# Kernel tuning notes

Measured on AMD Instinct MI355X. Metric: run time of the kernel, lower is better.

Reference implementation:

```python
import jax, jax.numpy as jnp
import numpy as np
from jax import lax

TF_ALPHA = 0.125


def _teacher_force(z, x, alpha):
    # z: (B, dz), x: (B, dx); force first dx dims of z where x is not NaN
    dx = x.shape[-1]
    head = z[:, :dx]
    forced = jnp.where(jnp.isnan(x), head, alpha * x + (1.0 - alpha) * head)
    return jnp.concatenate([forced, z[:, dx:]], axis=-1)


def setup_inputs() -> dict:
    key = jax.random.key(0)
    ks = jax.random.split(key, 8)
    B, T, dx, dz, dh, ds = 256, 1024, 64, 128, 512, 16
    X = jax.random.normal(ks[0], (B, T, dx), dtype=jnp.float32)
    inputs = jax.random.normal(ks[1], (B, T, ds), dtype=jnp.float32)
    # A in (0, 0.9) for stable linear part; small weight scales to avoid blowup over T steps
    A = jax.random.uniform(ks[2], (B, dz), dtype=jnp.float32) * 0.9
    W1 = jax.random.normal(ks[3], (B, dz, dh), dtype=jnp.float32) * (0.5 / np.sqrt(dh))
    W2 = jax.random.normal(ks[4], (B, dh, dz), dtype=jnp.float32) * (0.5 / np.sqrt(dz))
    h1 = jax.random.normal(ks[5], (B, dz), dtype=jnp.float32) * 0.1
    h2 = jax.random.normal(ks[6], (B, dh), dtype=jnp.float32) * 0.1
    C = jax.random.normal(ks[7], (B, dz, ds), dtype=jnp.float32) * (0.5 / np.sqrt(ds))
    return {"X": X, "inputs": inputs, "A": A, "W1": W1, "W2": W2,
            "h1": h1, "h2": h2, "C": C}


def _plrnn_forward(X, inputs, A, W1, W2, h1, h2, C):
    B, T, dx = X.shape
    dz = A.shape[-1]
    # z0 = zeros teacher-forced with alpha=1 from X[:, 0]
    z0 = jnp.zeros((B, dz), dtype=X.dtype)
    z0 = _teacher_force(z0, X[:, 0], alpha=1.0)

    Xt = jnp.transpose(X, (1, 0, 2))        # (T, B, dx)
    St = jnp.transpose(inputs, (1, 0, 2))   # (T, B, ds)

    def step(z, xs):
        x_t, s_t = xs
        zf = _teacher_force(z, x_t, TF_ALPHA)
        pre = jnp.einsum('bhz,bz->bh', W2, zf) + h2          # (B, dh)
        z_new = (A * zf
                 + jnp.einsum('bzh,bh->bz', W1, jax.nn.relu(pre))
                 + h1
                 + jnp.einsum('bzs,bs->bz', C, s_t))
        return z_new, z_new

    _, Z = lax.scan(step, z0, (Xt, St))      # Z: (T, B, dz)
    Z = jnp.transpose(Z, (1, 0, 2))          # (B, T, dz)
    return Z[:, :, :dx]                      # dim_x_proj == 0 path


def reference(X, inputs, A, W1, W2, h1, h2, C):
    return _plrnn_forward(X, inputs, A, W1, W2, h1, h2, C)
```

## Files before the change

### kernel.cpp

```cpp
#include <hip/hip_runtime.h>
#include <math.h>


#define NB 256
#define T  1024
#define DX 64
#define DZ 128
#define DH 512
#define DS 16
#define CHUNK 128

typedef _Float16 half8 __attribute__((ext_vector_type(8)));
typedef _Float16 v4h   __attribute__((ext_vector_type(4)));
typedef float    f32x4 __attribute__((ext_vector_type(4)));

__device__ __forceinline__ half8 cvt8(const float* __restrict__ src) {
  const float4 a = *reinterpret_cast<const float4*>(src);
  const float4 c = *reinterpret_cast<const float4*>(src + 4);
  half8 h;
  h[0] = (_Float16)a.x; h[1] = (_Float16)a.y; h[2] = (_Float16)a.z; h[3] = (_Float16)a.w;
  h[4] = (_Float16)c.x; h[5] = (_Float16)c.y; h[6] = (_Float16)c.z; h[7] = (_Float16)c.w;
  return h;
}

__global__ __launch_bounds__(512, 2) void plrnn_kernel(
    const float* __restrict__ X, const float* __restrict__ S,
    const float* __restrict__ A, const float* __restrict__ W1,
    const float* __restrict__ W2, const float* __restrict__ h1,
    const float* __restrict__ h2, const float* __restrict__ C,
    float* __restrict__ out)
{
  __shared__ __align__(16) _Float16 zf_h[DZ];
  __shared__ __align__(16) _Float16 rt[DH];
  __shared__ __align__(16) float    Xc[CHUNK][DX];
  __shared__ __align__(16) float    Sc[CHUNK][DS];
  __shared__ __align__(16) float    outc[CHUNK][DX];

  const int b   = blockIdx.x;
  const int tid = threadIdx.x;
  const int w   = tid >> 6;
  const int l   = tid & 63;
  const int g   = l >> 4;
  const int r15 = l & 15;

  {
    #pragma unroll
    for (int k = 0; k < 4; ++k) {
      const int flat = k * 2048 + tid * 4;
      int srow = 1 + (flat >> 6);
      if (srow > T - 1) srow = T - 1;
      const float4 v = *reinterpret_cast<const float4*>(X + ((size_t)b * T + srow) * DX + (flat & 63));
      *reinterpret_cast<float4*>(&((float*)Xc)[flat]) = v;
    }
    const int flat = tid * 4;
    const float4 v = *reinterpret_cast<const float4*>(S + ((size_t)b * T) * DS + flat);
    *reinterpret_cast<float4*>(&((float*)Sc)[flat]) = v;
  }

  half8 w2f[4][4];
  #pragma unroll
  for (int mt = 0; mt < 4; ++mt)
    #pragma unroll
    for (int kt = 0; kt < 4; ++kt)
      w2f[mt][kt] = cvt8(W2 + ((size_t)b * DH + 64 * w + 16 * mt + r15) * DZ + 32 * kt + 8 * g);

  half8 w1f[16];
  #pragma unroll
  for (int j = 0; j < 16; ++j) {
    const int kt = (2 * w + j) & 15;
    w1f[j] = cvt8(W1 + ((size_t)b * DZ + 16 * w + r15) * DH + 32 * kt + 8 * g);
  }

  half8 w1ft;
  #pragma unroll
  for (int e = 0; e < 8; ++e) w1ft[e] = (_Float16)0.0f;
  {
    const int row = 16 * w + r15;
    if (g == 0)      w1ft = cvt8(C + ((size_t)b * DZ + row) * DS + 0);
    else if (g == 1) w1ft = cvt8(C + ((size_t)b * DZ + row) * DS + 8);
  }

  f32x4 h2v[4];
  #pragma unroll
  for (int mt = 0; mt < 4; ++mt)
    h2v[mt] = *reinterpret_cast<const f32x4*>(h2 + (size_t)b * DH + 64 * w + 16 * mt + 4 * g);

  f32x4 Areg = {0.f, 0.f, 0.f, 0.f}, h1reg = {0.f, 0.f, 0.f, 0.f};
  f32x4 zfcur = {0.f, 0.f, 0.f, 0.f};
  if (r15 == 0) {
    Areg  = *reinterpret_cast<const f32x4*>(A  + (size_t)b * DZ + 16 * w + 4 * g);
    h1reg = *reinterpret_cast<const f32x4*>(h1 + (size_t)b * DZ + 16 * w + 4 * g);
    if (w < 4) {
      const f32x4 x0 = *reinterpret_cast<const f32x4*>(X + ((size_t)b * T) * DX + 16 * w + 4 * g);
      #pragma unroll
      for (int j = 0; j < 4; ++j) zfcur[j] = (x0[j] != x0[j]) ? 0.f : x0[j];
    }
    v4h zp;
    #pragma unroll
    for (int j = 0; j < 4; ++j) zp[j] = (_Float16)zfcur[j];
    *reinterpret_cast<v4h*>(&zf_h[16 * w + 4 * g]) = zp;
  }
  __syncthreads();

  const f32x4 zero4 = {0.f, 0.f, 0.f, 0.f};

  for (int t = 0; t < T; ++t) {
    if ((t & (CHUNK - 1)) == 0 && t) {
      const int c0 = t - CHUNK;
      #pragma unroll
      for (int k = 0; k < 4; ++k) {
        const int flat = k * 2048 + tid * 4;
        const float4 v = *reinterpret_cast<const float4*>(&((float*)outc)[flat]);
        *reinterpret_cast<float4*>(out + ((size_t)b * T + c0) * DX + flat) = v;
      }
      #pragma unroll
      for (int k = 0; k < 4; ++k) {
        const int flat = k * 2048 + tid * 4;
        int srow = t + 1 + (flat >> 6);
        if (srow > T - 1) srow = T - 1;
        const float4 v = *reinterpret_cast<const float4*>(X + ((size_t)b * T + srow) * DX + (flat & 63));
        *reinterpret_cast<float4*>(&((float*)Xc)[flat]) = v;
      }
      {
        const int flat = tid * 4;
        const float4 v = *reinterpret_cast<const float4*>(S + ((size_t)b * T + t) * DS + flat);
        *reinterpret_cast<float4*>(&((float*)Sc)[flat]) = v;
      }
      __syncthreads();
    }
    const int tc = t & (CHUNK - 1);

    const f32x4 xv  = *reinterpret_cast<const f32x4*>(&Xc[tc][16 * (w & 3) + 4 * g]);
    const f32x4 sa0 = *reinterpret_cast<const f32x4*>(&Sc[tc][8 * (g & 1)]);
    const f32x4 sa1 = *reinterpret_cast<const f32x4*>(&Sc[tc][8 * (g & 1) + 4]);
    half8 brt;
    #pragma unroll
    for (int e = 0; e < 4; ++e) {
      brt[e]     = (g < 2) ? (_Float16)sa0[e] : (_Float16)0.0f;
      brt[e + 4] = (g < 2) ? (_Float16)sa1[e] : (_Float16)0.0f;
    }
    const f32x4 tailv = __builtin_amdgcn_mfma_f32_16x16x32_f16(w1ft, brt, zero4, 0, 0, 0);

    half8 bz[4];
    #pragma unroll
    for (int kt = 0; kt < 4; ++kt)
      bz[kt] = *reinterpret_cast<const half8*>(zf_h + 32 * kt + 8 * g);

    f32x4 acc1[4];
    #pragma unroll
    for (int mt = 0; mt < 4; ++mt)
      acc1[mt] = __builtin_amdgcn_mfma_f32_16x16x32_f16(w2f[mt][0], bz[0], h2v[mt], 0, 0, 0);
    #pragma unroll
    for (int kt = 1; kt < 4; ++kt)
      #pragma unroll
      for (int mt = 0; mt < 4; ++mt)
        acc1[mt] = __builtin_amdgcn_mfma_f32_16x16x32_f16(w2f[mt][kt], bz[kt], acc1[mt], 0, 0, 0);

    if (r15 == 0) {
      #pragma unroll
      for (int mt = 0; mt < 4; ++mt) {
        v4h p;
        p[0] = (_Float16)fmaxf(acc1[mt][0], 0.f);
        p[1] = (_Float16)fmaxf(acc1[mt][1], 0.f);
        p[2] = (_Float16)fmaxf(acc1[mt][2], 0.f);
        p[3] = (_Float16)fmaxf(acc1[mt][3], 0.f);
        *reinterpret_cast<v4h*>(&rt[64 * w + 16 * mt + 4 * g]) = p;
      }
    }

    f32x4 acc2[8];
    {
      const half8 br0 = *reinterpret_cast<const half8*>(rt + 64 * w + 8 * g);
      const half8 br1 = *reinterpret_cast<const half8*>(rt + 64 * w + 32 + 8 * g);
      acc2[0] = __builtin_amdgcn_mfma_f32_16x16x32_f16(w1f[0], br0, tailv, 0, 0, 0);
      acc2[1] = __builtin_amdgcn_mfma_f32_16x16x32_f16(w1f[1], br1, zero4, 0, 0, 0);
    }
    __syncthreads();

    #pragma unroll
    for (int j = 2; j < 8; ++j) {
      const half8 br = *reinterpret_cast<const half8*>(rt + 32 * ((2 * w + j) & 15) + 8 * g);
      acc2[j] = __builtin_amdgcn_mfma_f32_16x16x32_f16(w1f[j], br, zero4, 0, 0, 0);
    }
    #pragma unroll
    for (int j = 8; j < 16; ++j) {
      const half8 br = *reinterpret_cast<const half8*>(rt + 32 * ((2 * w + j) & 15) + 8 * g);
      acc2[j - 8] = __builtin_amdgcn_mfma_f32_16x16x32_f16(w1f[j], br, acc2[j - 8], 0, 0, 0);
    }

    if (r15 == 0) {
      const f32x4 u = ((acc2[0] + acc2[1]) + (acc2[2] + acc2[3]))
                    + ((acc2[4] + acc2[5]) + (acc2[6] + acc2[7]));
      f32x4 zn, zfn;
      #pragma unroll
      for (int j = 0; j < 4; ++j) zn[j] = Areg[j] * zfcur[j] + u[j] + h1reg[j];
      zfn = zn;
      if (w < 4) {
        #pragma unroll
        for (int j = 0; j < 4; ++j)
          zfn[j] = (xv[j] != xv[j]) ? zn[j] : (0.125f * xv[j] + 0.875f * zn[j]);
      }
      zfcur = zfn;
      v4h zp;
      #pragma unroll
      for (int j = 0; j < 4; ++j) zp[j] = (_Float16)zfn[j];
      *reinterpret_cast<v4h*>(&zf_h[16 * w + 4 * g]) = zp;
      if (w < 4)
        *reinterpret_cast<f32x4*>(&outc[tc][16 * w + 4 * g]) = zn;
    }
    __syncthreads();
  }

  {
    const int c0 = T - CHUNK;
    #pragma unroll
    for (int k = 0; k < 4; ++k) {
      const int flat = k * 2048 + tid * 4;
      const float4 v = *reinterpret_cast<const float4*>(&((float*)outc)[flat]);
      *reinterpret_cast<float4*>(out + ((size_t)b * T + c0) * DX + flat) = v;
    }
  }
}

extern "C" void kernel_launch(void* const* d_in, const int* in_sizes, int n_in,
                              void* d_out, int out_size, void* d_ws, size_t ws_size,
                              hipStream_t stream) {
  const float* X  = (const float*)d_in[0];
  const float* S  = (const float*)d_in[1];
  const float* A  = (const float*)d_in[2];
  const float* W1 = (const float*)d_in[3];
  const float* W2 = (const float*)d_in[4];
  const float* h1 = (const float*)d_in[5];
  const float* h2 = (const float*)d_in[6];
  const float* C  = (const float*)d_in[7];
  float* out = (float*)d_out;
  plrnn_kernel<<<dim3(NB), dim3(512), 0, stream>>>(X, S, A, W1, W2, h1, h2, C, out);
}
```

Before: 1.157 ms.

## Specialize warps: four compute W2 stage, four compute W1 stage

Splits the 8 warps into two roles. Warps 0-3 hold all of W2 and compute the pre-activation and ReLU. Warps 4-7 hold all of W1 and compute the output update, the C·s tail, and h1, which is folded into the tail MFMA through a constant-one input lane. The aim is to drop the duplicated small per-warp work and reduce MFMA dependency stalls, since each warp now runs longer independent chains. The cost is that only half the warps are active in each phase of the step, so per-step latency may rise because the two stages are still serialized by barriers, and h1 is now rounded to fp16.

```diff
diff --git a/kernel.cpp b/kernel.cpp
--- a/kernel.cpp
+++ b/kernel.cpp
@@ -42,6 +42,8 @@
   const int l   = tid & 63;
   const int g   = l >> 4;
   const int r15 = l & 15;
+  const int p1w = (w < 4);
+  const int w2  = w & 3;
 
   {
     #pragma unroll
@@ -57,48 +59,62 @@
     *reinterpret_cast<float4*>(&((float*)Sc)[flat]) = v;
   }
 
-  half8 w2f[4][4];
+  half8 wf[32];
+  if (p1w) {
+    #pragma unroll
+    for (int mt = 0; mt < 8; ++mt)
+      #pragma unroll
+      for (int kt = 0; kt < 4; ++kt)
+        wf[mt * 4 + kt] = cvt8(W2 + ((size_t)b * DH + 128 * w2 + 16 * mt + r15) * DZ + 32 * kt + 8 * g);
+  } else {
+    #pragma unroll
+    for (int mt = 0; mt < 2; ++mt)
+      #pragma unroll
+      for (int kt = 0; kt < 16; ++kt)
+        wf[mt * 16 + kt] = cvt8(W1 + ((size_t)b * DZ + 32 * w2 + 16 * mt + r15) * DH + 32 * kt + 8 * g);
+  }
+
+  half8 tailf[2];
   #pragma unroll
-  for (int mt = 0; mt < 4; ++mt)
-    #pragma unroll
-    for (int kt = 0; kt < 4; ++kt)
-      w2f[mt][kt] = cvt8(W2 + ((size_t)b * DH + 64 * w + 16 * mt + r15) * DZ + 32 * kt + 8 * g);
-
-  half8 w1f[16];
+  for (int mt = 0; mt < 2; ++mt)
+    #pragma unroll
+    for (int e = 0; e < 8; ++e) tailf[mt][e] = (_Float16)0.0f;
+  if (!p1w) {
+    #pragma unroll
+    for (int mt = 0; mt < 2; ++mt) {
+      const int row = 32 * w2 + 16 * mt + r15;
+      if (g == 0)      tailf[mt] = cvt8(C + ((size_t)b * DZ + row) * DS + 0);
+      else if (g == 1) tailf[mt] = cvt8(C + ((size_t)b * DZ + row) * DS + 8);
+      else if (g == 2) tailf[mt][0] = (_Float16)h1[(size_t)b * DZ + row];
+    }
+  }
+
+  f32x4 hc[8];
   #pragma unroll
-  for (int j = 0; j < 16; ++j) {
-    const int kt = (2 * w + j) & 15;
-    w1f[j] = cvt8(W1 + ((size_t)b * DZ + 16 * w + r15) * DH + 32 * kt + 8 * g);
-  }
-
-  half8 w1ft;
-  #pragma unroll
-  for (int e = 0; e < 8; ++e) w1ft[e] = (_Float16)0.0f;
-  {
-    const int row = 16 * w + r15;
-    if (g == 0)      w1ft = cvt8(C + ((size_t)b * DZ + row) * DS + 0);
-    else if (g == 1) w1ft = cvt8(C + ((size_t)b * DZ + row) * DS + 8);
-  }
-
-  f32x4 h2v[4];
-  #pragma unroll
-  for (int mt = 0; mt < 4; ++mt)
-    h2v[mt] = *reinterpret_cast<const f32x4*>(h2 + (size_t)b * DH + 64 * w + 16 * mt + 4 * g);
-
-  f32x4 Areg = {0.f, 0.f, 0.f, 0.f}, h1reg = {0.f, 0.f, 0.f, 0.f};
-  f32x4 zfcur = {0.f, 0.f, 0.f, 0.f};
-  if (r15 == 0) {
-    Areg  = *reinterpret_cast<const f32x4*>(A  + (size_t)b * DZ + 16 * w + 4 * g);
-    h1reg = *reinterpret_cast<const f32x4*>(h1 + (size_t)b * DZ + 16 * w + 4 * g);
-    if (w < 4) {
-      const f32x4 x0 = *reinterpret_cast<const f32x4*>(X + ((size_t)b * T) * DX + 16 * w + 4 * g);
-      #pragma unroll
-      for (int j = 0; j < 4; ++j) zfcur[j] = (x0[j] != x0[j]) ? 0.f : x0[j];
-    }
-    v4h zp;
-    #pragma unroll
-    for (int j = 0; j < 4; ++j) zp[j] = (_Float16)zfcur[j];
-    *reinterpret_cast<v4h*>(&zf_h[16 * w + 4 * g]) = zp;
+  for (int i = 0; i < 8; ++i) hc[i] = (f32x4){0.f, 0.f, 0.f, 0.f};
+  if (p1w) {
+    #pragma unroll
+    for (int mt = 0; mt < 8; ++mt)
+      hc[mt] = *reinterpret_cast<const f32x4*>(h2 + (size_t)b * DH + 128 * w2 + 16 * mt + 4 * g);
+  } else {
+    #pragma unroll
+    for (int mt = 0; mt < 2; ++mt) {
+      const int row = 32 * w2 + 16 * mt + 4 * g;
+      hc[mt] = *reinterpret_cast<const f32x4*>(A + (size_t)b * DZ + row);
+      f32x4 zf0 = {0.f, 0.f, 0.f, 0.f};
+      if (row < DX) {
+        const f32x4 x0 = *reinterpret_cast<const f32x4*>(X + ((size_t)b * T) * DX + row);
+        #pragma unroll
+        for (int j = 0; j < 4; ++j) zf0[j] = (x0[j] != x0[j]) ? 0.f : x0[j];
+      }
+      hc[2 + mt] = zf0;
+      if (r15 == 0) {
+        v4h zp;
+        #pragma unroll
+        for (int j = 0; j < 4; ++j) zp[j] = (_Float16)zf0[j];
+        *reinterpret_cast<v4h*>(&zf_h[row]) = zp;
+      }
+    }
   }
   __syncthreads();
 
@@ -130,83 +146,99 @@
     }
     const int tc = t & (CHUNK - 1);
 
-    const f32x4 xv  = *reinterpret_cast<const f32x4*>(&Xc[tc][16 * (w & 3) + 4 * g]);
-    const f32x4 sa0 = *reinterpret_cast<const f32x4*>(&Sc[tc][8 * (g & 1)]);
-    const f32x4 sa1 = *reinterpret_cast<const f32x4*>(&Sc[tc][8 * (g & 1) + 4]);
-    half8 brt;
-    #pragma unroll
-    for (int e = 0; e < 4; ++e) {
-      brt[e]     = (g < 2) ? (_Float16)sa0[e] : (_Float16)0.0f;
-      brt[e + 4] = (g < 2) ? (_Float16)sa1[e] : (_Float16)0.0f;
-    }
-    const f32x4 tailv = __builtin_amdgcn_mfma_f32_16x16x32_f16(w1ft, brt, zero4, 0, 0, 0);
-
-    half8 bz[4];
-    #pragma unroll
-    for (int kt = 0; kt < 4; ++kt)
-      bz[kt] = *reinterpret_cast<const half8*>(zf_h + 32 * kt + 8 * g);
-
-    f32x4 acc1[4];
-    #pragma unroll
-    for (int mt = 0; mt < 4; ++mt)
-      acc1[mt] = __builtin_amdgcn_mfma_f32_16x16x32_f16(w2f[mt][0], bz[0], h2v[mt], 0, 0, 0);
-    #pragma unroll
-    for (int kt = 1; kt < 4; ++kt)
-      #pragma unroll
-      for (int mt = 0; mt < 4; ++mt)
-        acc1[mt] = __builtin_amdgcn_mfma_f32_16x16x32_f16(w2f[mt][kt], bz[kt], acc1[mt], 0, 0, 0);
-
-    if (r15 == 0) {
-      #pragma unroll
-      for (int mt = 0; mt < 4; ++mt) {
-        v4h p;
-        p[0] = (_Float16)fmaxf(acc1[mt][0], 0.f);
-        p[1] = (_Float16)fmaxf(acc1[mt][1], 0.f);
-        p[2] = (_Float16)fmaxf(acc1[mt][2], 0.f);
-        p[3] = (_Float16)fmaxf(acc1[mt][3], 0.f);
-        *reinterpret_cast<v4h*>(&rt[64 * w + 16 * mt + 4 * g]) = p;
-      }
-    }
-
-    f32x4 acc2[8];
-    {
-      const half8 br0 = *reinterpret_cast<const half8*>(rt + 64 * w + 8 * g);
-      const half8 br1 = *reinterpret_cast<const half8*>(rt + 64 * w + 32 + 8 * g);
-      acc2[0] = __builtin_amdgcn_mfma_f32_16x16x32_f16(w1f[0], br0, tailv, 0, 0, 0);
-      acc2[1] = __builtin_amdgcn_mfma_f32_16x16x32_f16(w1f[1], br1, zero4, 0, 0, 0);
+    f32x4 tacc[2];
+    f32x4 xva[2];
+
+    if (p1w) {
+      half8 bz[4];
+      #pragma unroll
+      for (int kt = 0; kt < 4; ++kt)
+        bz[kt] = *reinterpret_cast<const half8*>(zf_h + 32 * kt + 8 * g);
+
+      f32x4 acc1[8];
+      #pragma unroll
+      for (int mt = 0; mt < 8; ++mt)
+        acc1[mt] = __builtin_amdgcn_mfma_f32_16x16x32_f16(wf[mt * 4 + 0], bz[0], hc[mt], 0, 0, 0);
+      #pragma unroll
+      for (int kt = 1; kt < 4; ++kt)
+        #pragma unroll
+        for (int mt = 0; mt < 8; ++mt)
+          acc1[mt] = __builtin_amdgcn_mfma_f32_16x16x32_f16(wf[mt * 4 + kt], bz[kt], acc1[mt], 0, 0, 0);
+
+      if (r15 == 0) {
+        #pragma unroll
+        for (int mt = 0; mt < 8; ++mt) {
+          v4h p;
+          p[0] = (_Float16)fmaxf(acc1[mt][0], 0.f);
+          p[1] = (_Float16)fmaxf(acc1[mt][1], 0.f);
+          p[2] = (_Float16)fmaxf(acc1[mt][2], 0.f);
+          p[3] = (_Float16)fmaxf(acc1[mt][3], 0.f);
+          *reinterpret_cast<v4h*>(&rt[128 * w2 + 16 * mt + 4 * g]) = p;
+        }
+      }
+    } else {
+      half8 brt;
+      {
+        const f32x4 sa0 = *reinterpret_cast<const f32x4*>(&Sc[tc][8 * (g & 1)]);
+        const f32x4 sa1 = *reinterpret_cast<const f32x4*>(&Sc[tc][8 * (g & 1) + 4]);
+        #pragma unroll
+        for (int e = 0; e < 4; ++e) {
+          brt[e]     = (g < 2) ? (_Float16)sa0[e] : (_Float16)0.0f;
+          brt[e + 4] = (g < 2) ? (_Float16)sa1[e] : (_Float16)0.0f;
+        }
+        if (g == 2) brt[0] = (_Float16)1.0f;
+      }
+      #pragma unroll
+      for (int mt = 0; mt < 2; ++mt)
+        tacc[mt] = __builtin_amdgcn_mfma_f32_16x16x32_f16(tailf[mt], brt, zero4, 0, 0, 0);
+      if (w2 < 2) {
+        #pragma unroll
+        for (int mt = 0; mt < 2; ++mt)
+          xva[mt] = *reinterpret_cast<const f32x4*>(&Xc[tc][32 * w2 + 16 * mt + 4 * g]);
+      }
     }
     __syncthreads();
 
-    #pragma unroll
-    for (int j = 2; j < 8; ++j) {
-      const half8 br = *reinterpret_cast<const half8*>(rt + 32 * ((2 * w + j) & 15) + 8 * g);
-      acc2[j] = __builtin_amdgcn_mfma_f32_16x16x32_f16(w1f[j], br, zero4, 0, 0, 0);
-    }
-    #pragma unroll
-    for (int j = 8; j < 16; ++j) {
-      const half8 br = *reinterpret_cast<const half8*>(rt + 32 * ((2 * w + j) & 15) + 8 * g);
-      acc2[j - 8] = __builtin_amdgcn_mfma_f32_16x16x32_f16(w1f[j], br, acc2[j - 8], 0, 0, 0);
-    }
-
-    if (r15 == 0) {
-      const f32x4 u = ((acc2[0] + acc2[1]) + (acc2[2] + acc2[3]))
-                    + ((acc2[4] + acc2[5]) + (acc2[6] + acc2[7]));
-      f32x4 zn, zfn;
-      #pragma unroll
-      for (int j = 0; j < 4; ++j) zn[j] = Areg[j] * zfcur[j] + u[j] + h1reg[j];
-      zfn = zn;
-      if (w < 4) {
-        #pragma unroll
-        for (int j = 0; j < 4; ++j)
-          zfn[j] = (xv[j] != xv[j]) ? zn[j] : (0.125f * xv[j] + 0.875f * zn[j]);
-      }
-      zfcur = zfn;
-      v4h zp;
-      #pragma unroll
-      for (int j = 0; j < 4; ++j) zp[j] = (_Float16)zfn[j];
-      *reinterpret_cast<v4h*>(&zf_h[16 * w + 4 * g]) = zp;
-      if (w < 4)
-        *reinterpret_cast<f32x4*>(&outc[tc][16 * w + 4 * g]) = zn;
+    if (!p1w) {
+      f32x4 acc2[8];
+      #pragma unroll
+      for (int mt = 0; mt < 2; ++mt) {
+        acc2[mt * 4 + 0] = tacc[mt];
+        acc2[mt * 4 + 1] = zero4;
+        acc2[mt * 4 + 2] = zero4;
+        acc2[mt * 4 + 3] = zero4;
+      }
+      #pragma unroll
+      for (int kt = 0; kt < 16; ++kt) {
+        const half8 br = *reinterpret_cast<const half8*>(rt + 32 * kt + 8 * g);
+        acc2[0 * 4 + (kt & 3)] = __builtin_amdgcn_mfma_f32_16x16x32_f16(wf[0 * 16 + kt], br, acc2[0 * 4 + (kt & 3)], 0, 0, 0);
+        acc2[1 * 4 + (kt & 3)] = __builtin_amdgcn_mfma_f32_16x16x32_f16(wf[1 * 16 + kt], br, acc2[1 * 4 + (kt & 3)], 0, 0, 0);
+      }
+
+      if (r15 == 0) {
+        #pragma unroll
+        for (int mt = 0; mt < 2; ++mt) {
+          const int row = 32 * w2 + 16 * mt + 4 * g;
+          const f32x4 u = (acc2[mt * 4 + 0] + acc2[mt * 4 + 1])
+                        + (acc2[mt * 4 + 2] + acc2[mt * 4 + 3]);
+          f32x4 zn, zfn;
+          #pragma unroll
+          for (int j = 0; j < 4; ++j) zn[j] = hc[mt][j] * hc[2 + mt][j] + u[j];
+          zfn = zn;
+          if (w2 < 2) {
+            *reinterpret_cast<f32x4*>(&outc[tc][row]) = zn;
+            #pragma unroll
+            for (int j = 0; j < 4; ++j)
+              zfn[j] = (xva[mt][j] != xva[mt][j]) ? zn[j]
+                     : (0.125f * xva[mt][j] + 0.875f * zn[j]);
+          }
+          hc[2 + mt] = zfn;
+          v4h zp;
+          #pragma unroll
+          for (int j = 0; j < 4; ++j) zp[j] = (_Float16)zfn[j];
+          *reinterpret_cast<v4h*>(&zf_h[row]) = zp;
+        }
+      }
     }
     __syncthreads();
   }
```

Result: slower. 2.109 ms (+82.2%).
